# Kernel tuning notes

Hardware: AMD Instinct MI355X
Metric: run time of the kernel (lower is better)

The kernel has to match this reference:

```python
import jax, jax.numpy as jnp
import numpy as np

N_S, N_T, E, B = 100000, 100000, 4000000, 64
F_XS, F_XT, F_E, F_U, F_OUT = 10, 5, 10, 10, 5


def setup_inputs() -> dict:
    key = jax.random.key(0)
    ks = jax.random.split(key, 12)
    x_s = jax.random.normal(ks[0], (N_S, F_XS), dtype=jnp.float32)
    x_t = jax.random.normal(ks[1], (N_T, F_XT), dtype=jnp.float32)
    src = jax.random.randint(ks[2], (E,), 0, N_S)
    tgt = jax.random.randint(ks[3], (E,), 0, N_T)
    edge_index = jnp.stack([src, tgt], axis=0)
    edge_attr = jax.random.normal(ks[4], (E, F_E), dtype=jnp.float32)
    u = jax.random.normal(ks[5], (B, F_U), dtype=jnp.float32)
    batch_e = jax.random.randint(ks[6], (E,), 0, B)
    d_in = F_XS + F_XT + F_E + F_U  # 30
    # torch Linear default init: U(-1/sqrt(fan_in), 1/sqrt(fan_in))
    lim1 = 1.0 / np.sqrt(d_in)
    lim2 = 1.0 / np.sqrt(F_OUT)
    W1 = jax.random.uniform(ks[7], (d_in, F_OUT), minval=-lim1, maxval=lim1, dtype=jnp.float32)
    b1 = jax.random.uniform(ks[8], (F_OUT,), minval=-lim1, maxval=lim1, dtype=jnp.float32)
    W2 = jax.random.uniform(ks[9], (F_OUT, F_OUT), minval=-lim2, maxval=lim2, dtype=jnp.float32)
    b2 = jax.random.uniform(ks[10], (F_OUT,), minval=-lim2, maxval=lim2, dtype=jnp.float32)
    return {"x_s": x_s, "x_t": x_t, "edge_index": edge_index, "edge_attr": edge_attr,
            "u": u, "batch_e": batch_e, "W1": W1, "b1": b1, "W2": W2, "b2": b2}


def reference(x_s, x_t, edge_index, edge_attr, u, batch_e, W1, b1, W2, b2):
    src, tgt = edge_index[0], edge_index[1]
    # gather per-edge features and concat: [E, 30]
    feat = jnp.concatenate([x_s[src], x_t[tgt], edge_attr, u[batch_e]], axis=1)
    h = feat @ W1 + b1
    h = jax.nn.leaky_relu(h, negative_slope=0.1)
    out = h @ W2 + b2
    return out
```

## Files before the change

### kernel.cpp

```cpp
#include <hip/hip_runtime.h>

#define THREADS 256


__global__ __launch_bounds__(THREADS) void edge_model_kernel(
    const float* __restrict__ x_s,
    const float* __restrict__ x_t,
    const int* __restrict__ edge_index,
    const float* __restrict__ edge_attr,
    const float* __restrict__ u,
    const int* __restrict__ batch_e,
    const float* __restrict__ W1,
    const float* __restrict__ b1,
    const float* __restrict__ W2,
    const float* __restrict__ b2,
    float* __restrict__ out,
    int E)
{
    __shared__ float sW1[35 * 5];
    __shared__ float sb1[5];
    __shared__ float sW2[5 * 5];
    __shared__ float sb2[5];
    __shared__ float su[64 * 11];
    __shared__ float sout[THREADS * 5];

    const int t = threadIdx.x;

    for (int i = t; i < 35 * 5; i += THREADS) sW1[i] = W1[i];
    if (t < 5)  sb1[t] = b1[t];
    if (t < 25) sW2[t] = W2[t];
    if (t >= 32 && t < 37) sb2[t - 32] = b2[t - 32];
    for (int i = t; i < 64 * 10; i += THREADS) {
        int r = i / 10, c = i - r * 10;
        su[r * 11 + c] = u[i];
    }
    __syncthreads();

    const int e = blockIdx.x * THREADS + t;

    if (e < E) {
        const int src = edge_index[e];
        const int tgt = edge_index[E + e];
        const int b   = batch_e[e];

        float feat[35];

        const float2* xs2 = reinterpret_cast<const float2*>(x_s + (size_t)src * 10);
        #pragma unroll
        for (int i = 0; i < 5; ++i) {
            float2 v = xs2[i];
            feat[2 * i]     = v.x;
            feat[2 * i + 1] = v.y;
        }
        #pragma unroll
        for (int i = 0; i < 5; ++i) feat[10 + i] = x_t[(size_t)tgt * 5 + i];
        const float2* ea2 = reinterpret_cast<const float2*>(edge_attr + (size_t)e * 10);
        #pragma unroll
        for (int i = 0; i < 5; ++i) {
            float2 v = ea2[i];
            feat[15 + 2 * i] = v.x;
            feat[16 + 2 * i] = v.y;
        }
        #pragma unroll
        for (int i = 0; i < 10; ++i) feat[25 + i] = su[b * 11 + i];

        float h[5];
        #pragma unroll
        for (int j = 0; j < 5; ++j) {
            float acc = sb1[j];
            #pragma unroll
            for (int k = 0; k < 35; ++k) acc = fmaf(feat[k], sW1[k * 5 + j], acc);
            h[j] = (acc > 0.0f) ? acc : 0.1f * acc;
        }
        #pragma unroll
        for (int j = 0; j < 5; ++j) {
            float acc = sb2[j];
            #pragma unroll
            for (int i = 0; i < 5; ++i) acc = fmaf(h[i], sW2[i * 5 + j], acc);
            sout[t * 5 + j] = acc;
        }
    }
    __syncthreads();

    const size_t base  = (size_t)blockIdx.x * THREADS * 5;
    const int nvalid   = min(THREADS, E - blockIdx.x * THREADS);
    const int nfloats  = nvalid * 5;
    for (int i = t; i < nfloats; i += THREADS) out[base + i] = sout[i];
}

extern "C" void kernel_launch(void* const* d_in, const int* in_sizes, int n_in,
                              void* d_out, int out_size, void* d_ws, size_t ws_size,
                              hipStream_t stream)
{
    const float* x_s       = (const float*)d_in[0];
    const float* x_t       = (const float*)d_in[1];
    const int*   edge_idx  = (const int*)  d_in[2];
    const float* edge_attr = (const float*)d_in[3];
    const float* u         = (const float*)d_in[4];
    const int*   batch_e   = (const int*)  d_in[5];
    const float* W1        = (const float*)d_in[6];
    const float* b1        = (const float*)d_in[7];
    const float* W2        = (const float*)d_in[8];
    const float* b2        = (const float*)d_in[9];
    float*       out       = (float*)d_out;

    const int E = in_sizes[5];

    const int grid = (E + THREADS - 1) / THREADS;
    edge_model_kernel<<<grid, THREADS, 0, stream>>>(
        x_s, x_t, edge_idx, edge_attr, u, batch_e, W1, b1, W2, b2, out, E);
}
```

Measured before the change: 362.1 us.

## Process four edges per thread with vectorized nontemporal loads and stores

New measurement: 517.5 us. 1.43x slower.

```diff
diff --git a/kernel.cpp b/kernel.cpp
--- a/kernel.cpp
+++ b/kernel.cpp
@@ -1,6 +1,10 @@
 #include <hip/hip_runtime.h>
 
 #define THREADS 256
+#define EPT 4
+
+typedef float f32x4 __attribute__((ext_vector_type(4)));
+typedef int   i32x4 __attribute__((ext_vector_type(4)));
 
 
 __global__ __launch_bounds__(THREADS) void edge_model_kernel(
@@ -22,7 +26,6 @@
     __shared__ float sW2[5 * 5];
     __shared__ float sb2[5];
     __shared__ float su[64 * 11];
-    __shared__ float sout[THREADS * 5];
 
     const int t = threadIdx.x;
 
@@ -36,56 +39,125 @@
     }
     __syncthreads();
 
-    const int e = blockIdx.x * THREADS + t;
+    const int e0 = (blockIdx.x * THREADS + t) * EPT;
 
-    if (e < E) {
-        const int src = edge_index[e];
-        const int tgt = edge_index[E + e];
-        const int b   = batch_e[e];
+    if (e0 + EPT <= E) {
+        int src[EPT], tgt[EPT], bb[EPT];
+        {
+            i32x4 v = *reinterpret_cast<const i32x4*>(edge_index + e0);
+            src[0] = v.x; src[1] = v.y; src[2] = v.z; src[3] = v.w;
+        }
+        if ((E & 3) == 0) {
+            i32x4 v = *reinterpret_cast<const i32x4*>(edge_index + E + e0);
+            tgt[0] = v.x; tgt[1] = v.y; tgt[2] = v.z; tgt[3] = v.w;
+        } else {
+            #pragma unroll
+            for (int k = 0; k < EPT; ++k) tgt[k] = edge_index[E + e0 + k];
+        }
+        {
+            i32x4 v = *reinterpret_cast<const i32x4*>(batch_e + e0);
+            bb[0] = v.x; bb[1] = v.y; bb[2] = v.z; bb[3] = v.w;
+        }
 
-        float feat[35];
+        float eav[40];
+        {
+            const f32x4* ea4 = reinterpret_cast<const f32x4*>(edge_attr + (size_t)e0 * 10);
+            #pragma unroll
+            for (int i = 0; i < 10; ++i) {
+                f32x4 v = __builtin_nontemporal_load(ea4 + i);
+                eav[4 * i]     = v.x;
+                eav[4 * i + 1] = v.y;
+                eav[4 * i + 2] = v.z;
+                eav[4 * i + 3] = v.w;
+            }
+        }
 
-        const float2* xs2 = reinterpret_cast<const float2*>(x_s + (size_t)src * 10);
+        float2 xs[EPT][5];
+        float  xt[EPT][5];
+        #pragma unroll
+        for (int k = 0; k < EPT; ++k) {
+            const float2* p = reinterpret_cast<const float2*>(x_s + (size_t)src[k] * 10);
+            #pragma unroll
+            for (int i = 0; i < 5; ++i) xs[k][i] = p[i];
+        }
+        #pragma unroll
+        for (int k = 0; k < EPT; ++k) {
+            const float* p = x_t + (size_t)tgt[k] * 5;
+            #pragma unroll
+            for (int i = 0; i < 5; ++i) xt[k][i] = p[i];
+        }
+
+        float ov[EPT * 5];
+        #pragma unroll
+        for (int k = 0; k < EPT; ++k) {
+            float feat[35];
+            #pragma unroll
+            for (int i = 0; i < 5; ++i) {
+                feat[2 * i]     = xs[k][i].x;
+                feat[2 * i + 1] = xs[k][i].y;
+            }
+            #pragma unroll
+            for (int i = 0; i < 5; ++i) feat[10 + i] = xt[k][i];
+            #pragma unroll
+            for (int i = 0; i < 10; ++i) feat[15 + i] = eav[k * 10 + i];
+            #pragma unroll
+            for (int i = 0; i < 10; ++i) feat[25 + i] = su[bb[k] * 11 + i];
+
+            float h[5];
+            #pragma unroll
+            for (int j = 0; j < 5; ++j) {
+                float acc = sb1[j];
+                #pragma unroll
+                for (int kk = 0; kk < 35; ++kk) acc = fmaf(feat[kk], sW1[kk * 5 + j], acc);
+                h[j] = (acc > 0.0f) ? acc : 0.1f * acc;
+            }
+            #pragma unroll
+            for (int j = 0; j < 5; ++j) {
+                float acc = sb2[j];
+                #pragma unroll
+                for (int i = 0; i < 5; ++i) acc = fmaf(h[i], sW2[i * 5 + j], acc);
+                ov[k * 5 + j] = acc;
+            }
+        }
+
+        f32x4* o4 = reinterpret_cast<f32x4*>(out + (size_t)e0 * 5);
         #pragma unroll
         for (int i = 0; i < 5; ++i) {
-            float2 v = xs2[i];
-            feat[2 * i]     = v.x;
-            feat[2 * i + 1] = v.y;
+            f32x4 v;
+            v.x = ov[4 * i]; v.y = ov[4 * i + 1]; v.z = ov[4 * i + 2]; v.w = ov[4 * i + 3];
+            __builtin_nontemporal_store(v, o4 + i);
         }
-        #pragma unroll
-        for (int i = 0; i < 5; ++i) feat[10 + i] = x_t[(size_t)tgt * 5 + i];
-        const float2* ea2 = reinterpret_cast<const float2*>(edge_attr + (size_t)e * 10);
-        #pragma unroll
-        for (int i = 0; i < 5; ++i) {
-            float2 v = ea2[i];
-            feat[15 + 2 * i] = v.x;
-            feat[16 + 2 * i] = v.y;
-        }
-        #pragma unroll
-        for (int i = 0; i < 10; ++i) feat[25 + i] = su[b * 11 + i];
-
-        float h[5];
-        #pragma unroll
-        for (int j = 0; j < 5; ++j) {
-            float acc = sb1[j];
+    } else {
+        for (int e = e0; e < E; ++e) {
+            const int s  = edge_index[e];
+            const int tg = edge_index[E + e];
+            const int b  = batch_e[e];
+            float feat[35];
             #pragma unroll
-            for (int k = 0; k < 35; ++k) acc = fmaf(feat[k], sW1[k * 5 + j], acc);
-            h[j] = (acc > 0.0f) ? acc : 0.1f * acc;
-        }
-        #pragma unroll
-        for (int j = 0; j < 5; ++j) {
-            float acc = sb2[j];
+            for (int i = 0; i < 10; ++i) feat[i]      = x_s[(size_t)s * 10 + i];
             #pragma unroll
-            for (int i = 0; i < 5; ++i) acc = fmaf(h[i], sW2[i * 5 + j], acc);
-            sout[t * 5 + j] = acc;
+            for (int i = 0; i < 5; ++i)  feat[10 + i] = x_t[(size_t)tg * 5 + i];
+            #pragma unroll
+            for (int i = 0; i < 10; ++i) feat[15 + i] = edge_attr[(size_t)e * 10 + i];
+            #pragma unroll
+            for (int i = 0; i < 10; ++i) feat[25 + i] = su[b * 11 + i];
+            float h[5];
+            #pragma unroll
+            for (int j = 0; j < 5; ++j) {
+                float acc = sb1[j];
+                #pragma unroll
+                for (int kk = 0; kk < 35; ++kk) acc = fmaf(feat[kk], sW1[kk * 5 + j], acc);
+                h[j] = (acc > 0.0f) ? acc : 0.1f * acc;
+            }
+            #pragma unroll
+            for (int j = 0; j < 5; ++j) {
+                float acc = sb2[j];
+                #pragma unroll
+                for (int i = 0; i < 5; ++i) acc = fmaf(h[i], sW2[i * 5 + j], acc);
+                out[(size_t)e * 5 + j] = acc;
+            }
         }
     }
-    __syncthreads();
-
-    const size_t base  = (size_t)blockIdx.x * THREADS * 5;
-    const int nvalid   = min(THREADS, E - blockIdx.x * THREADS);
-    const int nfloats  = nvalid * 5;
-    for (int i = t; i < nfloats; i += THREADS) out[base + i] = sout[i];
 }
 
 extern "C" void kernel_launch(void* const* d_in, const int* in_sizes, int n_in,
@@ -106,7 +178,8 @@
 
     const int E = in_sizes[5];
 
-    const int grid = (E + THREADS - 1) / THREADS;
+    const int edges_per_block = THREADS * EPT;
+    const int grid = (E + edges_per_block - 1) / edges_per_block;
     edge_model_kernel<<<grid, THREADS, 0, stream>>>(
         x_s, x_t, edge_idx, edge_attr, u, batch_e, W1, b1, W2, b2, out, E);
 }
```

## Stage edge features through shared memory with cooperative coalesced gathers

Applied to the files above, without the earlier changes.

Result: slower. 411.5 us (+13.6%).

```diff
diff --git a/kernel.cpp b/kernel.cpp
--- a/kernel.cpp
+++ b/kernel.cpp
@@ -1,9 +1,11 @@
 #include <hip/hip_runtime.h>
 
 #define THREADS 256
+#define EPB 256
+#define FSTRIDE 27
 
 
-__global__ __launch_bounds__(THREADS) void edge_model_kernel(
+__global__ __launch_bounds__(THREADS, 4) void edge_model_kernel(
     const float* __restrict__ x_s,
     const float* __restrict__ x_t,
     const int* __restrict__ edge_index,
@@ -19,12 +21,17 @@
 {
     __shared__ float sW1[35 * 5];
     __shared__ float sb1[5];
-    __shared__ float sW2[5 * 5];
+    __shared__ float sW2[25];
     __shared__ float sb2[5];
     __shared__ float su[64 * 11];
-    __shared__ float sout[THREADS * 5];
+    __shared__ int   ssrc[EPB];
+    __shared__ int   stgt[EPB];
+    __shared__ float sfeat[EPB * FSTRIDE];
+    __shared__ float sout[EPB * 5];
 
-    const int t = threadIdx.x;
+    const int t    = threadIdx.x;
+    const int base = blockIdx.x * EPB;
+    const int nval = min(EPB, E - base);
 
     for (int i = t; i < 35 * 5; i += THREADS) sW1[i] = W1[i];
     if (t < 5)  sb1[t] = b1[t];
@@ -34,58 +41,76 @@
         int r = i / 10, c = i - r * 10;
         su[r * 11 + c] = u[i];
     }
+
+    int myb = 0;
+    if (t < nval) {
+        ssrc[t] = edge_index[base + t];
+        stgt[t] = edge_index[(size_t)E + base + t];
+        myb     = batch_e[base + t];
+    }
     __syncthreads();
 
-    const int e = blockIdx.x * THREADS + t;
 
-    if (e < E) {
-        const int src = edge_index[e];
-        const int tgt = edge_index[E + e];
-        const int b   = batch_e[e];
+    {
+        const int tot = nval * 10;
+        for (int i = t; i < tot; i += THREADS) {
+            int e = i / 10, c = i - e * 10;
+            sfeat[e * FSTRIDE + c] = x_s[(size_t)ssrc[e] * 10 + c];
+        }
+    }
+    {
+        const int tot = nval * 5;
+        for (int i = t; i < tot; i += THREADS) {
+            int e = i / 5, c = i - e * 5;
+            sfeat[e * FSTRIDE + 10 + c] = x_t[(size_t)stgt[e] * 5 + c];
+        }
+    }
+    {
+        const int tot = nval * 10;
+        const float* ea = edge_attr + (size_t)base * 10;
+        for (int i = t; i < tot; i += THREADS) {
+            int e = i / 10, c = i - e * 10;
+            sfeat[e * FSTRIDE + 15 + c] = ea[i];
+        }
+    }
+    __syncthreads();
 
-        float feat[35];
-
-        const float2* xs2 = reinterpret_cast<const float2*>(x_s + (size_t)src * 10);
-        #pragma unroll
-        for (int i = 0; i < 5; ++i) {
-            float2 v = xs2[i];
-            feat[2 * i]     = v.x;
-            feat[2 * i + 1] = v.y;
-        }
-        #pragma unroll
-        for (int i = 0; i < 5; ++i) feat[10 + i] = x_t[(size_t)tgt * 5 + i];
-        const float2* ea2 = reinterpret_cast<const float2*>(edge_attr + (size_t)e * 10);
-        #pragma unroll
-        for (int i = 0; i < 5; ++i) {
-            float2 v = ea2[i];
-            feat[15 + 2 * i] = v.x;
-            feat[16 + 2 * i] = v.y;
-        }
-        #pragma unroll
-        for (int i = 0; i < 10; ++i) feat[25 + i] = su[b * 11 + i];
+    if (t < nval) {
+        const float* f  = &sfeat[t * FSTRIDE];
+        const float* uu = &su[myb * 11];
 
         float h[5];
         #pragma unroll
-        for (int j = 0; j < 5; ++j) {
-            float acc = sb1[j];
+        for (int j = 0; j < 5; ++j) h[j] = sb1[j];
+        #pragma unroll
+        for (int k = 0; k < 25; ++k) {
+            float v = f[k];
             #pragma unroll
-            for (int k = 0; k < 35; ++k) acc = fmaf(feat[k], sW1[k * 5 + j], acc);
-            h[j] = (acc > 0.0f) ? acc : 0.1f * acc;
+            for (int j = 0; j < 5; ++j) h[j] = fmaf(v, sW1[k * 5 + j], h[j]);
         }
+        #pragma unroll
+        for (int k = 0; k < 10; ++k) {
+            float v = uu[k];
+            #pragma unroll
+            for (int j = 0; j < 5; ++j) h[j] = fmaf(v, sW1[(25 + k) * 5 + j], h[j]);
+        }
+        #pragma unroll
+        for (int j = 0; j < 5; ++j) h[j] = (h[j] > 0.0f) ? h[j] : 0.1f * h[j];
+
         #pragma unroll
         for (int j = 0; j < 5; ++j) {
             float acc = sb2[j];
             #pragma unroll
-            for (int i = 0; i < 5; ++i) acc = fmaf(h[i], sW2[i * 5 + j], acc);
+            for (int i2 = 0; i2 < 5; ++i2) acc = fmaf(h[i2], sW2[i2 * 5 + j], acc);
             sout[t * 5 + j] = acc;
         }
     }
     __syncthreads();
 
-    const size_t base  = (size_t)blockIdx.x * THREADS * 5;
-    const int nvalid   = min(THREADS, E - blockIdx.x * THREADS);
-    const int nfloats  = nvalid * 5;
-    for (int i = t; i < nfloats; i += THREADS) out[base + i] = sout[i];
+    const int nflt = nval * 5;
+    float* ob = out + (size_t)base * 5;
+    for (int i = t; i < nflt; i += THREADS)
+        __builtin_nontemporal_store(sout[i], ob + i);
 }
 
 extern "C" void kernel_launch(void* const* d_in, const int* in_sizes, int n_in,
@@ -106,7 +131,7 @@
 
     const int E = in_sizes[5];
 
-    const int grid = (E + THREADS - 1) / THREADS;
+    const int grid = (E + EPB - 1) / EPB;
     edge_model_kernel<<<grid, THREADS, 0, stream>>>(
         x_s, x_t, edge_idx, edge_attr, u, batch_e, W1, b1, W2, b2, out, E);
 }
```
